# Kernel tuning notes

Hardware: AMD Instinct MI355X
Metric: run time of the kernel (lower is better)

The kernel has to match this reference:

```python
import jax, jax.numpy as jnp
import numpy as np

N = 1024
NEVAL = 131072
NUM_POLES = 8
DOMAIN = (-1.0, 1.0)
DOMAIN_LEN = DOMAIN[1] - DOMAIN[0]
EPS = 1e-14


def _cheb_nodes(n):
    # Chebyshev points of the second kind: cos(pi * linspace(0, 1, n))
    return jnp.cos(jnp.pi * jnp.linspace(0.0, 1.0, n))


def _to_standard(x):
    return 2.0 * (x - DOMAIN[0]) / DOMAIN_LEN - 1.0


def _barycentric_weights(nodes, poles_real, poles_imag):
    # Vectorized equivalent of the original per-node Python loop.
    n = nodes.shape[0]
    diff = nodes[:, None] - nodes[None, :]            # (N, N)
    eye = jnp.eye(n, dtype=bool)
    # log_weights[j] = -sum_{i!=j} log|nodes[j]-nodes[i]|
    log_w = -jnp.sum(jnp.log(jnp.where(eye, 1.0, jnp.abs(diff))), axis=1)
    # signs[j] = (-1)^(# of negative off-diagonal diffs); diagonal diff==0 contributes nothing
    neg_count = jnp.sum(diff < 0, axis=1)
    signs = jnp.where(neg_count % 2 == 0, 1.0, -1.0)
    # each conjugate pole pair contributes 2*log(sqrt((x-r)^2 + i^2)) = log((x-r)^2 + i^2)
    pole_term = jnp.log((nodes[:, None] - poles_real[None, :]) ** 2
                        + poles_imag[None, :] ** 2)   # (N, M)
    log_w = log_w + jnp.sum(pole_term, axis=1)
    log_w = log_w - jnp.max(log_w)
    w = signs * jnp.exp(log_w)
    return w / jnp.abs(w[0])


def setup_inputs() -> dict:
    key = jax.random.key(0)
    k1, k2, k3, k4 = jax.random.split(key, 4)
    x_eval = jax.random.uniform(k1, (NEVAL,), dtype=jnp.float32)  # in [0,1) subset of domain
    values = jax.random.normal(k2, (N,), dtype=jnp.float32)
    poles_real = jax.random.normal(k3, (NUM_POLES,), dtype=jnp.float32)
    poles_imag = jax.random.normal(k4, (NUM_POLES,), dtype=jnp.float32)
    return {"x_eval": x_eval, "values": values,
            "poles_real": poles_real, "poles_imag": poles_imag}


def reference(x_eval, values, poles_real, poles_imag):
    nodes = _cheb_nodes(N)
    nodes_std = _to_standard(nodes)                   # identity for domain (-1,1)
    w = _barycentric_weights(nodes, poles_real, poles_imag)

    x_std = _to_standard(x_eval)
    d_x = x_std[None, :] - nodes_std[:, None]         # (N, NEVAL)
    small = jnp.abs(d_x) < EPS
    small_any = jnp.any(small, axis=0)                # (NEVAL,)
    d_safe = jnp.where(small, 1.0, d_x)
    inv = jnp.where(small_any[None, :], 0.0, 1.0 / d_safe)
    inv = jnp.where(small, 1.0, inv)                  # exact-hit columns: indicator row -> 1

    num = jnp.einsum('n,nm,n->m', values, inv, w)
    den = jnp.einsum('nm,n->m', inv, w)
    return num / den
```

## Files before the change

kernel.cpp:

```cpp
#include <hip/hip_runtime.h>
#include <math.h>

#define N_NODES 1024
#define N_EVAL 131072
#define NUM_POLES 8
#define PI_D 3.14159265358979323846


__global__ __launch_bounds__(256) void setup_kernel(
    const float* __restrict__ values,
    const float* __restrict__ poles_real,
    const float* __restrict__ poles_imag,
    float* __restrict__ ws) {
    const int j = blockIdx.x * 256 + threadIdx.x;
    const double nd = cos(PI_D * (double)j / (double)(N_NODES - 1));
    double prod = (j == 0 || j == N_NODES - 1) ? 0.5 : 1.0;
#pragma unroll
    for (int m = 0; m < NUM_POLES; ++m) {
        const double dr = nd - (double)poles_real[m];
        const double di = (double)poles_imag[m];
        prod *= dr * dr + di * di;
    }
    if (j & 1) prod = -prod;
    ws[j]        = (float)nd;
    ws[j + 1024] = (float)prod;
    ws[j + 2048] = (float)(prod * (double)values[j]);
}

__global__ __launch_bounds__(256, 8) void eval_scalar_kernel(
    const float* __restrict__ x_eval,
    const float* __restrict__ ws,
    float* __restrict__ out) {
    __shared__ float2 s_red[4][64];

    const int t = threadIdx.x;
    const int lane = t & 63;
    const int wid = __builtin_amdgcn_readfirstlane(t >> 6);
    const int pbase = blockIdx.x * 64;

    const float x = x_eval[pbase + lane];

    const float* __restrict__ nn = ws + wid * 256;
    const float* __restrict__ wq = ws + 1024 + wid * 256;
    const float* __restrict__ vq = ws + 2048 + wid * 256;

    float a0 = 0.0f, b0 = 0.0f, a1 = 0.0f, b1 = 0.0f;

#pragma unroll 2
    for (int j = 0; j < 256; j += 8) {
#pragma unroll
        for (int k = 0; k < 8; k += 2) {
            const float n0 = nn[j + k];
            const float w0 = wq[j + k];
            const float v0 = vq[j + k];
            const float n1 = nn[j + k + 1];
            const float w1 = wq[j + k + 1];
            const float v1 = vq[j + k + 1];
            const float d0 = x - n0;
            const float d1 = x - n1;
            const float r0 = __builtin_amdgcn_rcpf(d0);
            const float r1 = __builtin_amdgcn_rcpf(d1);
            a0 = fmaf(v0, r0, a0);
            b0 = fmaf(w0, r0, b0);
            a1 = fmaf(v1, r1, a1);
            b1 = fmaf(w1, r1, b1);
        }
    }

    s_red[wid][lane] = make_float2(a0 + a1, b0 + b1);
    __syncthreads();

    if (t < 64) {
        float num = 0.0f, den = 0.0f;
#pragma unroll
        for (int w = 0; w < 4; ++w) {
            const float2 p = s_red[w][t];
            num += p.x;
            den += p.y;
        }
        float res = num / den;
        if (__builtin_expect(__builtin_isnan(res), 0)) {
            const float xx = x_eval[pbase + t];
            float hn = 0.0f, hd = 0.0f;
            for (int jj = 0; jj < N_NODES; ++jj) {
                if (ws[jj] == xx) { hn += ws[2048 + jj]; hd += ws[1024 + jj]; }
            }
            res = hn / hd;
        }
        out[pbase + t] = res;
    }
}

__global__ __launch_bounds__(512, 4) void eval_kernel_fused(
    const float* __restrict__ x_eval,
    const float* __restrict__ values,
    const float* __restrict__ poles_real,
    const float* __restrict__ poles_imag,
    float* __restrict__ out) {
    __shared__ __align__(16) float s_n[N_NODES];
    __shared__ __align__(16) float s_w[N_NODES];
    __shared__ __align__(16) float s_v[N_NODES];
    __shared__ float2 s_r[8][256];

    const int t = threadIdx.x;

#pragma unroll
    for (int h = 0; h < 2; ++h) {
        const int j = t + h * 512;
        const double nd = cos(PI_D * (double)j / (double)(N_NODES - 1));
        double prod = (j == 0 || j == N_NODES - 1) ? 0.5 : 1.0;
#pragma unroll
        for (int m = 0; m < NUM_POLES; ++m) {
            const double dr = nd - (double)poles_real[m];
            const double di = (double)poles_imag[m];
            prod *= dr * dr + di * di;
        }
        if (j & 1) prod = -prod;
        s_n[j] = (float)nd;
        s_w[j] = (float)prod;
        s_v[j] = (float)(prod * (double)values[j]);
    }
    __syncthreads();

    const int lane = t & 63;
    const int wid  = t >> 6;
    const int pbase = blockIdx.x * 256;
    const float x0 = x_eval[pbase + lane];
    const float x1 = x_eval[pbase + 64 + lane];
    const float x2 = x_eval[pbase + 128 + lane];
    const float x3 = x_eval[pbase + 192 + lane];

    const float4* n4 = (const float4*)s_n + wid * 32;
    const float4* w4 = (const float4*)s_w + wid * 32;
    const float4* v4 = (const float4*)s_v + wid * 32;

    float a0 = 0.0f, b0 = 0.0f, a1 = 0.0f, b1 = 0.0f;
    float a2 = 0.0f, b2 = 0.0f, a3 = 0.0f, b3 = 0.0f;

#define NODE(C)                                                            \
    {                                                                      \
        const float d0 = x0 - an.C;                                        \
        const float d1 = x1 - an.C;                                        \
        const float d2 = x2 - an.C;                                        \
        const float d3 = x3 - an.C;                                        \
        const float r0 = __builtin_amdgcn_rcpf(d0);                        \
        const float r1 = __builtin_amdgcn_rcpf(d1);                        \
        const float r2 = __builtin_amdgcn_rcpf(d2);                        \
        const float r3 = __builtin_amdgcn_rcpf(d3);                        \
        a0 = fmaf(av.C, r0, a0); b0 = fmaf(aw.C, r0, b0);                  \
        a1 = fmaf(av.C, r1, a1); b1 = fmaf(aw.C, r1, b1);                  \
        a2 = fmaf(av.C, r2, a2); b2 = fmaf(aw.C, r2, b2);                  \
        a3 = fmaf(av.C, r3, a3); b3 = fmaf(aw.C, r3, b3);                  \
    }

#pragma unroll 4
    for (int q = 0; q < 32; ++q) {
        const float4 an = n4[q];
        const float4 aw = w4[q];
        const float4 av = v4[q];
        NODE(x) NODE(y) NODE(z) NODE(w)
    }
#undef NODE

    s_r[wid][lane]       = make_float2(a0, b0);
    s_r[wid][lane + 64]  = make_float2(a1, b1);
    s_r[wid][lane + 128] = make_float2(a2, b2);
    s_r[wid][lane + 192] = make_float2(a3, b3);
    __syncthreads();

    if (t < 256) {
        float nn = 0.0f, dd = 0.0f;
#pragma unroll
        for (int w = 0; w < 8; ++w) {
            const float2 pr = s_r[w][t];
            nn += pr.x;
            dd += pr.y;
        }
        float res = nn / dd;
        if (__builtin_expect(__builtin_isnan(res), 0)) {
            const float x = x_eval[pbase + t];
            float hn = 0.0f, hd = 0.0f;
            for (int j = 0; j < N_NODES; ++j) {
                if (s_n[j] == x) { hn += s_v[j]; hd += s_w[j]; }
            }
            res = hn / hd;
        }
        out[pbase + t] = res;
    }
}

extern "C" void kernel_launch(void* const* d_in, const int* in_sizes, int n_in,
                              void* d_out, int out_size, void* d_ws, size_t ws_size,
                              hipStream_t stream) {
    const float* x_eval     = (const float*)d_in[0];
    const float* values     = (const float*)d_in[1];
    const float* poles_real = (const float*)d_in[2];
    const float* poles_imag = (const float*)d_in[3];
    float* out = (float*)d_out;

    if (ws_size >= 3 * N_NODES * sizeof(float)) {
        float* ws = (float*)d_ws;
        setup_kernel<<<N_NODES / 256, 256, 0, stream>>>(values, poles_real,
                                                        poles_imag, ws);
        eval_scalar_kernel<<<N_EVAL / 64, 256, 0, stream>>>(x_eval, ws, out);
    } else {
        eval_kernel_fused<<<N_EVAL / 256, 512, 0, stream>>>(
            x_eval, values, poles_real, poles_imag, out);
    }
}
```

Baseline: 116.4 us.

## Hold node data in registers and rotate eval points across lanes systolically

Each lane now keeps 16 nodes with their weights and scaled values in registers. The evaluation point and its partial sums rotate around the 64-lane wavefront via shuffles, so every wave covers all 1024 nodes for its 64 points. This drops the per-node scalar memory loads and the cross-wave LDS reduction and __syncthreads. In exchange it adds five cross-lane shuffles per 16 nodes and more register pressure. The launch_bounds occupancy hint is also removed.

```diff
diff --git a/kernel.cpp b/kernel.cpp
--- a/kernel.cpp
+++ b/kernel.cpp
@@ -27,68 +27,76 @@
     ws[j + 2048] = (float)(prod * (double)values[j]);
 }
 
-__global__ __launch_bounds__(256, 8) void eval_scalar_kernel(
+__global__ __launch_bounds__(256) void eval_systolic_kernel(
     const float* __restrict__ x_eval,
     const float* __restrict__ ws,
     float* __restrict__ out) {
-    __shared__ float2 s_red[4][64];
-
     const int t = threadIdx.x;
     const int lane = t & 63;
-    const int wid = __builtin_amdgcn_readfirstlane(t >> 6);
-    const int pbase = blockIdx.x * 64;
-
-    const float x = x_eval[pbase + lane];
-
-    const float* __restrict__ nn = ws + wid * 256;
-    const float* __restrict__ wq = ws + 1024 + wid * 256;
-    const float* __restrict__ vq = ws + 2048 + wid * 256;
-
-    float a0 = 0.0f, b0 = 0.0f, a1 = 0.0f, b1 = 0.0f;
+    const int wid  = t >> 6;
+    const int pbase = (blockIdx.x * 4 + wid) * 64;
+
+    float n[16], w[16], v[16];
+    {
+        const float4* n4 = (const float4*)(ws)        + lane * 4;
+        const float4* w4 = (const float4*)(ws + 1024) + lane * 4;
+        const float4* v4 = (const float4*)(ws + 2048) + lane * 4;
+#pragma unroll
+        for (int q = 0; q < 4; ++q) {
+            const float4 a = n4[q];
+            const float4 b = w4[q];
+            const float4 c = v4[q];
+            n[q * 4 + 0] = a.x; n[q * 4 + 1] = a.y;
+            n[q * 4 + 2] = a.z; n[q * 4 + 3] = a.w;
+            w[q * 4 + 0] = b.x; w[q * 4 + 1] = b.y;
+            w[q * 4 + 2] = b.z; w[q * 4 + 3] = b.w;
+            v[q * 4 + 0] = c.x; v[q * 4 + 1] = c.y;
+            v[q * 4 + 2] = c.z; v[q * 4 + 3] = c.w;
+        }
+    }
+
+    float xr = x_eval[pbase + lane];
+    float aE = 0.0f, bE = 0.0f, aO = 0.0f, bO = 0.0f;
+    const int src = (lane + 1) & 63;
 
 #pragma unroll 2
-    for (int j = 0; j < 256; j += 8) {
-#pragma unroll
-        for (int k = 0; k < 8; k += 2) {
-            const float n0 = nn[j + k];
-            const float w0 = wq[j + k];
-            const float v0 = vq[j + k];
-            const float n1 = nn[j + k + 1];
-            const float w1 = wq[j + k + 1];
-            const float v1 = vq[j + k + 1];
-            const float d0 = x - n0;
-            const float d1 = x - n1;
-            const float r0 = __builtin_amdgcn_rcpf(d0);
-            const float r1 = __builtin_amdgcn_rcpf(d1);
-            a0 = fmaf(v0, r0, a0);
-            b0 = fmaf(w0, r0, b0);
-            a1 = fmaf(v1, r1, a1);
-            b1 = fmaf(w1, r1, b1);
-        }
-    }
-
-    s_red[wid][lane] = make_float2(a0 + a1, b0 + b1);
-    __syncthreads();
-
-    if (t < 64) {
-        float num = 0.0f, den = 0.0f;
-#pragma unroll
-        for (int w = 0; w < 4; ++w) {
-            const float2 p = s_red[w][t];
-            num += p.x;
-            den += p.y;
-        }
-        float res = num / den;
-        if (__builtin_expect(__builtin_isnan(res), 0)) {
-            const float xx = x_eval[pbase + t];
-            float hn = 0.0f, hd = 0.0f;
-            for (int jj = 0; jj < N_NODES; ++jj) {
-                if (ws[jj] == xx) { hn += ws[2048 + jj]; hd += ws[1024 + jj]; }
-            }
-            res = hn / hd;
-        }
-        out[pbase + t] = res;
-    }
+    for (int s = 0; s < 64; ++s) {
+#pragma unroll
+        for (int k = 0; k < 8; ++k) {
+            const float d = xr - n[k];
+            const float r = __builtin_amdgcn_rcpf(d);
+            aE = fmaf(v[k], r, aE);
+            bE = fmaf(w[k], r, bE);
+        }
+        const float aEn = __shfl(aE, src);
+        const float bEn = __shfl(bE, src);
+
+        float d8[8];
+#pragma unroll
+        for (int k = 0; k < 8; ++k) d8[k] = xr - n[8 + k];
+        const float xn = __shfl(xr, src);
+#pragma unroll
+        for (int k = 0; k < 8; ++k) {
+            const float r = __builtin_amdgcn_rcpf(d8[k]);
+            aO = fmaf(v[8 + k], r, aO);
+            bO = fmaf(w[8 + k], r, bO);
+        }
+        const float aOn = __shfl(aO, src);
+        const float bOn = __shfl(bO, src);
+
+        aE = aEn; bE = bEn; aO = aOn; bO = bOn; xr = xn;
+    }
+
+    float res = (aE + aO) / (bE + bO);
+    if (__builtin_expect(__builtin_isnan(res), 0)) {
+        const float xv = x_eval[pbase + lane];
+        float hn = 0.0f, hd = 0.0f;
+        for (int jj = 0; jj < N_NODES; ++jj) {
+            if (ws[jj] == xv) { hn += ws[2048 + jj]; hd += ws[1024 + jj]; }
+        }
+        res = hn / hd;
+    }
+    out[pbase + lane] = res;
 }
 
 __global__ __launch_bounds__(512, 4) void eval_kernel_fused(
@@ -202,7 +210,7 @@
         float* ws = (float*)d_ws;
         setup_kernel<<<N_NODES / 256, 256, 0, stream>>>(values, poles_real,
                                                         poles_imag, ws);
-        eval_scalar_kernel<<<N_EVAL / 64, 256, 0, stream>>>(x_eval, ws, out);
+        eval_systolic_kernel<<<N_EVAL / 256, 256, 0, stream>>>(x_eval, ws, out);
     } else {
         eval_kernel_fused<<<N_EVAL / 256, 512, 0, stream>>>(
             x_eval, values, poles_real, poles_imag, out);
```

New measurement: 126.9 us. +9.0%, slower.

## Broadcast node data via readlane from registers instead of scalar loads

Applied to the files above, without the earlier changes.

The eval kernel now has each wave load its 512-node slice of node, weight and value arrays into VGPRs once, 8 per lane. Inside the loop it broadcasts each node with v_readlane into SGPRs instead of issuing scalar memory loads. Each thread now handles two evaluation points, and blocks shrink to 128 threads split into 2 node halves. The aim is to take scalar-cache load latency out of the inner loop and reuse each node across two points. The cost is three readlane instructions per node, which could limit VALU throughput, and fewer waves per block.

```diff
diff --git a/kernel.cpp b/kernel.cpp
--- a/kernel.cpp
+++ b/kernel.cpp
@@ -27,63 +27,83 @@
     ws[j + 2048] = (float)(prod * (double)values[j]);
 }
 
-__global__ __launch_bounds__(256, 8) void eval_scalar_kernel(
+__global__ __launch_bounds__(128) void eval_readlane_kernel(
     const float* __restrict__ x_eval,
     const float* __restrict__ ws,
     float* __restrict__ out) {
-    __shared__ float2 s_red[4][64];
+    __shared__ float2 s_red[2][128];
 
     const int t = threadIdx.x;
     const int lane = t & 63;
-    const int wid = __builtin_amdgcn_readfirstlane(t >> 6);
-    const int pbase = blockIdx.x * 64;
-
-    const float x = x_eval[pbase + lane];
-
-    const float* __restrict__ nn = ws + wid * 256;
-    const float* __restrict__ wq = ws + 1024 + wid * 256;
-    const float* __restrict__ vq = ws + 2048 + wid * 256;
+    const int wid  = t >> 6;
+    const int pbase = blockIdx.x * 128;
+    const int nb = wid * 512;
+
+    float n0, n1, n2, n3, n4, n5, n6, n7;
+    float w0, w1, w2, w3, w4, w5, w6, w7;
+    float v0, v1, v2, v3, v4, v5, v6, v7;
+    {
+        const float4* np = (const float4*)(ws + nb)        + lane * 2;
+        const float4* wp = (const float4*)(ws + 1024 + nb) + lane * 2;
+        const float4* vp = (const float4*)(ws + 2048 + nb) + lane * 2;
+        const float4 na = np[0], nbq = np[1];
+        const float4 wa = wp[0], wb  = wp[1];
+        const float4 va = vp[0], vb  = vp[1];
+        n0 = na.x;  n1 = na.y;  n2 = na.z;  n3 = na.w;
+        n4 = nbq.x; n5 = nbq.y; n6 = nbq.z; n7 = nbq.w;
+        w0 = wa.x;  w1 = wa.y;  w2 = wa.z;  w3 = wa.w;
+        w4 = wb.x;  w5 = wb.y;  w6 = wb.z;  w7 = wb.w;
+        v0 = va.x;  v1 = va.y;  v2 = va.z;  v3 = va.w;
+        v4 = vb.x;  v5 = vb.y;  v6 = vb.z;  v7 = vb.w;
+    }
+    asm volatile("" : "+v"(n0), "+v"(n1), "+v"(n2), "+v"(n3),
+                      "+v"(n4), "+v"(n5), "+v"(n6), "+v"(n7));
+    asm volatile("" : "+v"(w0), "+v"(w1), "+v"(w2), "+v"(w3),
+                      "+v"(w4), "+v"(w5), "+v"(w6), "+v"(w7));
+    asm volatile("" : "+v"(v0), "+v"(v1), "+v"(v2), "+v"(v3),
+                      "+v"(v4), "+v"(v5), "+v"(v6), "+v"(v7));
+
+    const float x0 = x_eval[pbase + lane];
+    const float x1 = x_eval[pbase + 64 + lane];
 
     float a0 = 0.0f, b0 = 0.0f, a1 = 0.0f, b1 = 0.0f;
 
+#define NODE(NK, WK, VK)                                                     \
+    {                                                                        \
+        const float sn = __int_as_float(                                     \
+            __builtin_amdgcn_readlane(__float_as_int(NK), ow));              \
+        const float sw = __int_as_float(                                     \
+            __builtin_amdgcn_readlane(__float_as_int(WK), ow));              \
+        const float sv = __int_as_float(                                     \
+            __builtin_amdgcn_readlane(__float_as_int(VK), ow));              \
+        const float d0 = x0 - sn;                                            \
+        const float d1 = x1 - sn;                                            \
+        const float r0 = __builtin_amdgcn_rcpf(d0);                          \
+        const float r1 = __builtin_amdgcn_rcpf(d1);                          \
+        a0 = fmaf(sv, r0, a0); b0 = fmaf(sw, r0, b0);                        \
+        a1 = fmaf(sv, r1, a1); b1 = fmaf(sw, r1, b1);                        \
+    }
+
 #pragma unroll 2
-    for (int j = 0; j < 256; j += 8) {
-#pragma unroll
-        for (int k = 0; k < 8; k += 2) {
-            const float n0 = nn[j + k];
-            const float w0 = wq[j + k];
-            const float v0 = vq[j + k];
-            const float n1 = nn[j + k + 1];
-            const float w1 = wq[j + k + 1];
-            const float v1 = vq[j + k + 1];
-            const float d0 = x - n0;
-            const float d1 = x - n1;
-            const float r0 = __builtin_amdgcn_rcpf(d0);
-            const float r1 = __builtin_amdgcn_rcpf(d1);
-            a0 = fmaf(v0, r0, a0);
-            b0 = fmaf(w0, r0, b0);
-            a1 = fmaf(v1, r1, a1);
-            b1 = fmaf(w1, r1, b1);
-        }
-    }
-
-    s_red[wid][lane] = make_float2(a0 + a1, b0 + b1);
+    for (int ow = 0; ow < 64; ++ow) {
+        NODE(n0, w0, v0) NODE(n1, w1, v1) NODE(n2, w2, v2) NODE(n3, w3, v3)
+        NODE(n4, w4, v4) NODE(n5, w5, v5) NODE(n6, w6, v6) NODE(n7, w7, v7)
+    }
+#undef NODE
+
+    s_red[wid][lane]      = make_float2(a0, b0);
+    s_red[wid][lane + 64] = make_float2(a1, b1);
     __syncthreads();
 
-    if (t < 64) {
-        float num = 0.0f, den = 0.0f;
-#pragma unroll
-        for (int w = 0; w < 4; ++w) {
-            const float2 p = s_red[w][t];
-            num += p.x;
-            den += p.y;
-        }
-        float res = num / den;
+    if (t < 128) {
+        const float2 p0 = s_red[0][t];
+        const float2 p1 = s_red[1][t];
+        float res = (p0.x + p1.x) / (p0.y + p1.y);
         if (__builtin_expect(__builtin_isnan(res), 0)) {
-            const float xx = x_eval[pbase + t];
+            const float xv = x_eval[pbase + t];
             float hn = 0.0f, hd = 0.0f;
             for (int jj = 0; jj < N_NODES; ++jj) {
-                if (ws[jj] == xx) { hn += ws[2048 + jj]; hd += ws[1024 + jj]; }
+                if (ws[jj] == xv) { hn += ws[2048 + jj]; hd += ws[1024 + jj]; }
             }
             res = hn / hd;
         }
@@ -202,7 +222,7 @@
         float* ws = (float*)d_ws;
         setup_kernel<<<N_NODES / 256, 256, 0, stream>>>(values, poles_real,
                                                         poles_imag, ws);
-        eval_scalar_kernel<<<N_EVAL / 64, 256, 0, stream>>>(x_eval, ws, out);
+        eval_readlane_kernel<<<N_EVAL / 128, 128, 0, stream>>>(x_eval, ws, out);
     } else {
         eval_kernel_fused<<<N_EVAL / 256, 512, 0, stream>>>(
             x_eval, values, poles_real, poles_imag, out);
```

Result: slower. 133.2 us (+14.4%).

## Combine node pairs into one reciprocal and use packed float2 math

Applied to the files above, without the earlier changes.

The eval kernel now merges each pair of nodes into a single fraction, (v0*d1 + v1*d0)/(d0*d1). This halves the number of reciprocal instructions, which are transcendental-rate ops. The arithmetic is written with float2 vector types so the compiler can emit packed FMA/add/mul, and each thread evaluates two points. A new setup kernel writes duplicated, pre-negated pair coefficients into the workspace. In exchange, the product d0*d1 can overflow or underflow and lose accuracy near the nodes, the exact-hit fallback now depends on a NaN appearing from the product, and an extra launch is added.

```diff
diff --git a/kernel.cpp b/kernel.cpp
--- a/kernel.cpp
+++ b/kernel.cpp
@@ -5,6 +5,8 @@
 #define N_EVAL 131072
 #define NUM_POLES 8
 #define PI_D 3.14159265358979323846
+
+typedef float v2f __attribute__((ext_vector_type(2)));
 
 
 __global__ __launch_bounds__(256) void setup_kernel(
@@ -27,63 +29,88 @@
     ws[j + 2048] = (float)(prod * (double)values[j]);
 }
 
-__global__ __launch_bounds__(256, 8) void eval_scalar_kernel(
+__global__ __launch_bounds__(256) void setup_pairs_kernel(float* __restrict__ ws) {
+    const int k = blockIdx.x * 256 + threadIdx.x;
+    const float a   = ws[2 * k];
+    const float b   = ws[2 * k + 1];
+    const float w0  = ws[1024 + 2 * k];
+    const float w1  = ws[1024 + 2 * k + 1];
+    const float wv0 = ws[2048 + 2 * k];
+    const float wv1 = ws[2048 + 2 * k + 1];
+    float2* p = (float2*)(ws + 3072) + k * 6;
+    p[0] = make_float2(-a, -a);
+    p[1] = make_float2(-b, -b);
+    p[2] = make_float2(wv0, wv0);
+    p[3] = make_float2(wv1, wv1);
+    p[4] = make_float2(w0, w0);
+    p[5] = make_float2(w1, w1);
+}
+
+__global__ __launch_bounds__(256) void eval_pk_kernel(
     const float* __restrict__ x_eval,
     const float* __restrict__ ws,
     float* __restrict__ out) {
-    __shared__ float2 s_red[4][64];
+    __shared__ float2 s_rA[4][64];
+    __shared__ float2 s_rB[4][64];
 
     const int t = threadIdx.x;
     const int lane = t & 63;
     const int wid = __builtin_amdgcn_readfirstlane(t >> 6);
-    const int pbase = blockIdx.x * 64;
-
-    const float x = x_eval[pbase + lane];
-
-    const float* __restrict__ nn = ws + wid * 256;
-    const float* __restrict__ wq = ws + 1024 + wid * 256;
-    const float* __restrict__ vq = ws + 2048 + wid * 256;
-
-    float a0 = 0.0f, b0 = 0.0f, a1 = 0.0f, b1 = 0.0f;
-
-#pragma unroll 2
-    for (int j = 0; j < 256; j += 8) {
-#pragma unroll
-        for (int k = 0; k < 8; k += 2) {
-            const float n0 = nn[j + k];
-            const float w0 = wq[j + k];
-            const float v0 = vq[j + k];
-            const float n1 = nn[j + k + 1];
-            const float w1 = wq[j + k + 1];
-            const float v1 = vq[j + k + 1];
-            const float d0 = x - n0;
-            const float d1 = x - n1;
-            const float r0 = __builtin_amdgcn_rcpf(d0);
-            const float r1 = __builtin_amdgcn_rcpf(d1);
-            a0 = fmaf(v0, r0, a0);
-            b0 = fmaf(w0, r0, b0);
-            a1 = fmaf(v1, r1, a1);
-            b1 = fmaf(w1, r1, b1);
-        }
-    }
-
-    s_red[wid][lane] = make_float2(a0 + a1, b0 + b1);
+    const int pbase = blockIdx.x * 128;
+
+    v2f X;
+    X.x = x_eval[pbase + lane];
+    X.y = x_eval[pbase + 64 + lane];
+
+    const v2f* __restrict__ pc = (const v2f*)(ws + 3072) + wid * (128 * 6);
+
+    v2f A0 = {0.0f, 0.0f}, B0 = {0.0f, 0.0f};
+    v2f A1 = {0.0f, 0.0f}, B1 = {0.0f, 0.0f};
+
+#define PAIR(KK, AA, BB)                                                     \
+    {                                                                        \
+        const v2f* c = pc + (KK) * 6;                                        \
+        const v2f D0 = X + c[0];                         \
+        const v2f D1 = X + c[1];                                  \
+        const v2f Q  = D0 * D1;                                  \
+        v2f R;                                                               \
+        R.x = __builtin_amdgcn_rcpf(Q.x);                                    \
+        R.y = __builtin_amdgcn_rcpf(Q.y);                                    \
+        const v2f Nv = __builtin_elementwise_fma(c[2], D1, c[3] * D0);       \
+        const v2f Nw = __builtin_elementwise_fma(c[4], D1, c[5] * D0);       \
+        AA = __builtin_elementwise_fma(Nv, R, AA);                           \
+        BB = __builtin_elementwise_fma(Nw, R, BB);                           \
+    }
+
+#pragma unroll 4
+    for (int k = 0; k < 128; k += 2) {
+        PAIR(k, A0, B0)
+        PAIR(k + 1, A1, B1)
+    }
+#undef PAIR
+
+    const v2f A = A0 + A1;
+    const v2f B = B0 + B1;
+    s_rA[wid][lane] = make_float2(A.x, B.x);
+    s_rB[wid][lane] = make_float2(A.y, B.y);
     __syncthreads();
 
-    if (t < 64) {
+    if (t < 128) {
+        const int half = t >> 6;
+        const int idx  = t & 63;
         float num = 0.0f, den = 0.0f;
 #pragma unroll
         for (int w = 0; w < 4; ++w) {
-            const float2 p = s_red[w][t];
+            const float2 p = half ? s_rB[w][idx] : s_rA[w][idx];
             num += p.x;
             den += p.y;
         }
         float res = num / den;
         if (__builtin_expect(__builtin_isnan(res), 0)) {
-            const float xx = x_eval[pbase + t];
+            const float xv = x_eval[pbase + t];
             float hn = 0.0f, hd = 0.0f;
             for (int jj = 0; jj < N_NODES; ++jj) {
-                if (ws[jj] == xx) { hn += ws[2048 + jj]; hd += ws[1024 + jj]; }
+                if (ws[jj] == xv) { hn += ws[2048 + jj]; hd += ws[1024 + jj]; }
             }
             res = hn / hd;
         }
@@ -198,11 +225,12 @@
     const float* poles_imag = (const float*)d_in[3];
     float* out = (float*)d_out;
 
-    if (ws_size >= 3 * N_NODES * sizeof(float)) {
+    if (ws_size >= (3072 + 512 * 12) * sizeof(float)) {
         float* ws = (float*)d_ws;
         setup_kernel<<<N_NODES / 256, 256, 0, stream>>>(values, poles_real,
                                                         poles_imag, ws);
-        eval_scalar_kernel<<<N_EVAL / 64, 256, 0, stream>>>(x_eval, ws, out);
+        setup_pairs_kernel<<<2, 256, 0, stream>>>(ws);
+        eval_pk_kernel<<<N_EVAL / 128, 256, 0, stream>>>(x_eval, ws, out);
     } else {
         eval_kernel_fused<<<N_EVAL / 256, 512, 0, stream>>>(
             x_eval, values, poles_real, poles_imag, out);
```

New measurement: 135.8 us. +16.6%, slower.
